# Kernel tuning notes

Measured on AMD Instinct MI355X. Metric: run time of the kernel, lower is better.

## Reference

```python
import jax, jax.numpy as jnp
import numpy as np

B, S, IN_DIM, OUT_DIM = 4, 8192, 1024, 1024


def setup_inputs() -> dict:
    key = jax.random.key(0)
    kx, km, kv, kt = jax.random.split(key, 4)
    x = jax.random.normal(kx, (B, S, IN_DIM), dtype=jnp.float32)
    visual_mask = jax.random.randint(km, (B, S), 0, 2) > 0  # bool [B, S]
    # nn.Linear(in_dim, out_dim, bias=False): weight shape [out_dim, in_dim]
    bound = 1.0 / np.sqrt(IN_DIM)
    W_v = jax.random.uniform(kv, (OUT_DIM, IN_DIM), dtype=jnp.float32, minval=-bound, maxval=bound)
    W_t = jax.random.uniform(kt, (OUT_DIM, IN_DIM), dtype=jnp.float32, minval=-bound, maxval=bound)
    return {"x": x, "visual_mask": visual_mask, "W_v": W_v, "W_t": W_t}


def reference(x, visual_mask, W_v, W_t):
    # out = linear_v(x) * mask + linear_t(x) * ~mask
    y_v = jnp.einsum("bsd,od->bso", x, W_v)  # [B, S, OUT_DIM]
    y_t = jnp.einsum("bsd,od->bso", x, W_t)
    m = visual_mask[:, :, None]  # [B, S, 1]
    return jnp.where(m, y_v, y_t)
```

## Files before the change

### kernel.cpp

```cpp
#include <hip/hip_runtime.h>
#include <hip/hip_bf16.h>
#include <stdint.h>

#define M_TOT  32768
#define K_DIM  1024
#define N_DIM  1024

typedef short bf16x8 __attribute__((ext_vector_type(8)));
typedef float f32x4  __attribute__((ext_vector_type(4)));

#define AS1(p) ((__attribute__((address_space(1))) void*)(p))
#define AS3(p) ((__attribute__((address_space(3))) void*)(p))

__device__ __forceinline__ uint32_t packbf2(float a, float b) {
    __hip_bfloat162 h = __float22bfloat162_rn(make_float2(a, b));
    union { __hip_bfloat162 h; uint32_t u; } cvt;
    cvt.h = h;
    return cvt.u;
}

__global__ __launch_bounds__(1024) void prep_kernel(
        const float* __restrict__ x,  const int* __restrict__ mask,
        const float* __restrict__ wv, const float* __restrict__ wt,
        ushort* __restrict__ xb, ushort* __restrict__ dv, ushort* __restrict__ dt,
        int* __restrict__ V, int* __restrict__ T, int* __restrict__ cnt) {
    const int b   = blockIdx.x;
    const int tid = threadIdx.x;

    if (b < 32) {
        const int lane = tid & 63;
        const int wv_i = tid >> 6;

        int pre = 0;
        const int nPre4 = b * 256;
        for (int i = tid; i < nPre4; i += 1024) {
            int4 v = ((const int4*)mask)[i];
            pre += (v.x != 0) + (v.y != 0) + (v.z != 0) + (v.w != 0);
        }
#pragma unroll
        for (int d = 32; d > 0; d >>= 1) pre += __shfl_down(pre, d);
        __shared__ int wsum[16];
        __shared__ int pref_s;
        if (lane == 0) wsum[wv_i] = pre;
        __syncthreads();
        if (tid == 0) {
            int s = 0;
#pragma unroll
            for (int i = 0; i < 16; ++i) s += wsum[i];
            pref_s = s;
        }
        __syncthreads();
        const int prefix_v = pref_s;

        const int e   = b * 1024 + tid;
        const int bit = (mask[e] != 0) ? 1 : 0;
        unsigned long long bal = __ballot(bit);
        const int lexcl = __popcll(bal & ((1ull << lane) - 1ull));
        const int wcnt  = __popcll(bal);
        __shared__ int wc[16];
        if (lane == 0) wc[wv_i] = wcnt;
        __syncthreads();
        int wpre = 0;
        for (int i = 0; i < wv_i; ++i) wpre += wc[i];
        int chunk_tot = 0;
#pragma unroll
        for (int i = 0; i < 16; ++i) chunk_tot += wc[i];
        const int gv = prefix_v + wpre + lexcl;
        if (bit) V[gv]     = e;
        else     T[e - gv] = e;

        if (b == 31) {
            const int Nv = prefix_v + chunk_tot;
            const int Nt = M_TOT - Nv;
            if (tid == 0) { cnt[0] = Nv; cnt[1] = Nt; }
            const int NBv = (Nv + 127) >> 7, NBt = (Nt + 127) >> 7;
            for (int p = Nv + tid; p < NBv * 128; p += 1024) V[p] = -1;
            for (int p = Nt + tid; p < NBt * 128; p += 1024) T[p] = -1;
        }
        return;
    }

    if (b < 288) {
        int u = (b - 32) * 8192 + tid * 8;
        const float* src; ushort* dst; int off;
        if (u < 1048576) { src = wv; dst = dv; off = u; }
        else             { src = wt; dst = dt; off = u - 1048576; }
        float4 a0 = *(const float4*)(src + off);
        float4 a1 = *(const float4*)(src + off + 4);
        uint4 p;
        p.x = packbf2(a0.x, a0.y);
        p.y = packbf2(a0.z, a0.w);
        p.z = packbf2(a1.x, a1.y);
        p.w = packbf2(a1.z, a1.w);
        *(uint4*)(dst + off) = p;
        return;
    }

    const int off = (b - 288) * 8192 + tid * 8;
    float4 a0 = *(const float4*)(x + off);
    float4 a1 = *(const float4*)(x + off + 4);
    uint4 p;
    p.x = packbf2(a0.x, a0.y);
    p.y = packbf2(a0.z, a0.w);
    p.z = packbf2(a1.x, a1.y);
    p.w = packbf2(a1.z, a1.w);
    *(uint4*)(xb + off) = p;
}

__global__ __launch_bounds__(256) void gemm_kernel(
        const ushort* __restrict__ xb,
        const ushort* __restrict__ Wv,
        const ushort* __restrict__ Wt,
        const int*    __restrict__ V,
        const int*    __restrict__ T,
        const int*    __restrict__ cnt,
        float*        __restrict__ out) {
    __shared__ ushort sA[128 * 64];
    __shared__ ushort sB[128 * 64];

    const int tid  = threadIdx.x;
    const int lane = tid & 63;
    const int w    = tid >> 6;

    const int kx = blockIdx.x & 7;
    const int bn = (blockIdx.x >> 3) & 7;
    const int gk = blockIdx.x >> 6;
    const int bm = gk * 8 + kx;

    const int Nv  = cnt[0];
    const int Nt  = cnt[1];
    const int NBv = (Nv + 127) >> 7;
    const int NBt = (Nt + 127) >> 7;
    if (bm >= NBv + NBt) return;

    const bool vis = (bm < NBv);
    const int*    rowbase = vis ? (V + (size_t)bm * 128)
                                : (T + (size_t)(bm - NBv) * 128);
    const ushort* W       = vis ? Wv : Wt;
    const int n0 = bn * 128;

    const int trow = tid >> 3;
    const int kcb  = (tid & 7) ^ (trow & 7);
    const ushort* ap[4];
    const ushort* wp[4];
#pragma unroll
    for (int r = 0; r < 4; ++r) {
        int rr = rowbase[r * 32 + trow];
        if (rr < 0) rr = 0;
        ap[r] = xb + (size_t)rr * K_DIM + kcb * 8;
        wp[r] = W + (size_t)(n0 + r * 32 + trow) * K_DIM + kcb * 8;
    }

    const int ml   = lane & 15;
    const int quad = lane >> 4;
    const int wm = (w & 1) * 64;
    const int wn = (w >> 1) * 64;
    uint32_t aoff[2][4], boff[2][4];
#pragma unroll
    for (int ks = 0; ks < 2; ++ks) {
        int kxr = (ks * 4 + quad) ^ (ml & 7);
#pragma unroll
        for (int t = 0; t < 4; ++t) {
            aoff[ks][t] = (uint32_t)(((wm + t * 16 + ml) * 8 + kxr) * 16);
            boff[ks][t] = (uint32_t)(((wn + t * 16 + ml) * 8 + kxr) * 16);
        }
    }

    f32x4 acc[4][4];
#pragma unroll
    for (int i = 0; i < 4; ++i)
#pragma unroll
        for (int j = 0; j < 4; ++j) {
            f32x4 z = {0.f, 0.f, 0.f, 0.f};
            acc[i][j] = z;
        }

    char* sAb = (char*)sA;
    char* sBb = (char*)sB;

    for (int kt = 0; kt < 16; ++kt) {
        const int k0 = kt * 64;
#pragma unroll
        for (int r = 0; r < 4; ++r) {
            char* lb = sBb + (size_t)(r * 256 + w * 64) * 16;
            __builtin_amdgcn_global_load_lds(AS1(wp[r] + k0), AS3(lb), 16, 0, 0);
        }
#pragma unroll
        for (int r = 0; r < 4; ++r) {
            char* la = sAb + (size_t)(r * 256 + w * 64) * 16;
            __builtin_amdgcn_global_load_lds(AS1(ap[r] + k0), AS3(la), 16, 0, 0);
        }
        __syncthreads();
#pragma unroll
        for (int ks = 0; ks < 2; ++ks) {
            bf16x8 af[4], bf[4];
#pragma unroll
            for (int t = 0; t < 4; ++t) af[t] = *(const bf16x8*)(sAb + aoff[ks][t]);
#pragma unroll
            for (int t = 0; t < 4; ++t) bf[t] = *(const bf16x8*)(sBb + boff[ks][t]);
#pragma unroll
            for (int tm = 0; tm < 4; ++tm)
#pragma unroll
                for (int tn = 0; tn < 4; ++tn)
                    acc[tm][tn] = __builtin_amdgcn_mfma_f32_16x16x32_bf16(
                        af[tm], bf[tn], acc[tm][tn], 0, 0, 0);
        }
        __syncthreads();
    }

#pragma unroll
    for (int tm = 0; tm < 4; ++tm) {
        const int rb = wm + tm * 16 + quad * 4;
        int sr0 = rowbase[rb + 0];
        int sr1 = rowbase[rb + 1];
        int sr2 = rowbase[rb + 2];
        int sr3 = rowbase[rb + 3];
#pragma unroll
        for (int tn = 0; tn < 4; ++tn) {
            const int col = n0 + wn + tn * 16 + ml;
            if (sr0 >= 0) out[(size_t)sr0 * N_DIM + col] = acc[tm][tn][0];
            if (sr1 >= 0) out[(size_t)sr1 * N_DIM + col] = acc[tm][tn][1];
            if (sr2 >= 0) out[(size_t)sr2 * N_DIM + col] = acc[tm][tn][2];
            if (sr3 >= 0) out[(size_t)sr3 * N_DIM + col] = acc[tm][tn][3];
        }
    }
}

extern "C" void kernel_launch(void* const* d_in, const int* in_sizes, int n_in,
                              void* d_out, int out_size, void* d_ws, size_t ws_size,
                              hipStream_t stream) {
    const float* x    = (const float*)d_in[0];
    const int*   mask = (const int*)d_in[1];
    const float* Wv   = (const float*)d_in[2];
    const float* Wt   = (const float*)d_in[3];
    float* out = (float*)d_out;

    char* ws = (char*)d_ws;
    ushort* xb  = (ushort*)(ws);
    ushort* dWv = (ushort*)(ws + 67108864);
    ushort* dWt = (ushort*)(ws + 69206016);
    int* V   = (int*)(ws + 71303168);
    int* T   = V + 32768;
    int* cnt = T + 32768;

    prep_kernel<<<4384, 1024, 0, stream>>>(x, mask, Wv, Wt, xb, dWv, dWt, V, T, cnt);
    gemm_kernel<<<33 * 64, 256, 0, stream>>>(xb, dWv, dWt, V, T, cnt, out);
}
```

Before: 341.5 us.

## Fuse activation bf16 conversion into GEMM by loading fp32 x directly

After: 380.4 us. 11.4% more time.

```diff
diff --git a/kernel.cpp b/kernel.cpp
--- a/kernel.cpp
+++ b/kernel.cpp
@@ -20,9 +20,9 @@
 }
 
 __global__ __launch_bounds__(1024) void prep_kernel(
-        const float* __restrict__ x,  const int* __restrict__ mask,
+        const int* __restrict__ mask,
         const float* __restrict__ wv, const float* __restrict__ wt,
-        ushort* __restrict__ xb, ushort* __restrict__ dv, ushort* __restrict__ dt,
+        ushort* __restrict__ dv, ushort* __restrict__ dt,
         int* __restrict__ V, int* __restrict__ T, int* __restrict__ cnt) {
     const int b   = blockIdx.x;
     const int tid = threadIdx.x;
@@ -80,42 +80,29 @@
         return;
     }
 
-    if (b < 288) {
-        int u = (b - 32) * 8192 + tid * 8;
-        const float* src; ushort* dst; int off;
-        if (u < 1048576) { src = wv; dst = dv; off = u; }
-        else             { src = wt; dst = dt; off = u - 1048576; }
-        float4 a0 = *(const float4*)(src + off);
-        float4 a1 = *(const float4*)(src + off + 4);
-        uint4 p;
-        p.x = packbf2(a0.x, a0.y);
-        p.y = packbf2(a0.z, a0.w);
-        p.z = packbf2(a1.x, a1.y);
-        p.w = packbf2(a1.z, a1.w);
-        *(uint4*)(dst + off) = p;
-        return;
-    }
-
-    const int off = (b - 288) * 8192 + tid * 8;
-    float4 a0 = *(const float4*)(x + off);
-    float4 a1 = *(const float4*)(x + off + 4);
+    int u = (b - 32) * 8192 + tid * 8;
+    const float* src; ushort* dst; int off;
+    if (u < 1048576) { src = wv; dst = dv; off = u; }
+    else             { src = wt; dst = dt; off = u - 1048576; }
+    float4 a0 = *(const float4*)(src + off);
+    float4 a1 = *(const float4*)(src + off + 4);
     uint4 p;
     p.x = packbf2(a0.x, a0.y);
     p.y = packbf2(a0.z, a0.w);
     p.z = packbf2(a1.x, a1.y);
     p.w = packbf2(a1.z, a1.w);
-    *(uint4*)(xb + off) = p;
+    *(uint4*)(dst + off) = p;
 }
 
 __global__ __launch_bounds__(256) void gemm_kernel(
-        const ushort* __restrict__ xb,
+        const float*  __restrict__ x,
         const ushort* __restrict__ Wv,
         const ushort* __restrict__ Wt,
         const int*    __restrict__ V,
         const int*    __restrict__ T,
         const int*    __restrict__ cnt,
         float*        __restrict__ out) {
-    __shared__ ushort sA[128 * 64];
+    __shared__ float  sA[128 * 64];
     __shared__ ushort sB[128 * 64];
 
     const int tid  = threadIdx.x;
@@ -139,15 +126,20 @@
     const ushort* W       = vis ? Wv : Wt;
     const int n0 = bn * 128;
 
+    const int arow = tid >> 4;
+    const int akc  = (tid & 15) ^ arow;
+    const float* ap8[8];
+#pragma unroll
+    for (int r = 0; r < 8; ++r) {
+        int rr = rowbase[r * 16 + arow];
+        if (rr < 0) rr = 0;
+        ap8[r] = x + (size_t)rr * K_DIM + akc * 4;
+    }
     const int trow = tid >> 3;
     const int kcb  = (tid & 7) ^ (trow & 7);
-    const ushort* ap[4];
     const ushort* wp[4];
 #pragma unroll
     for (int r = 0; r < 4; ++r) {
-        int rr = rowbase[r * 32 + trow];
-        if (rr < 0) rr = 0;
-        ap[r] = xb + (size_t)rr * K_DIM + kcb * 8;
         wp[r] = W + (size_t)(n0 + r * 32 + trow) * K_DIM + kcb * 8;
     }
 
@@ -158,10 +150,11 @@
     uint32_t aoff[2][4], boff[2][4];
 #pragma unroll
     for (int ks = 0; ks < 2; ++ks) {
-        int kxr = (ks * 4 + quad) ^ (ml & 7);
+        const int kc0 = ks * 8 + quad * 2;
+        const int kxr = (ks * 4 + quad) ^ (ml & 7);
 #pragma unroll
         for (int t = 0; t < 4; ++t) {
-            aoff[ks][t] = (uint32_t)(((wm + t * 16 + ml) * 8 + kxr) * 16);
+            aoff[ks][t] = (uint32_t)(((wm + t * 16 + ml) * 16 + (kc0 ^ ml)) * 16);
             boff[ks][t] = (uint32_t)(((wn + t * 16 + ml) * 8 + kxr) * 16);
         }
     }
@@ -186,16 +179,25 @@
             __builtin_amdgcn_global_load_lds(AS1(wp[r] + k0), AS3(lb), 16, 0, 0);
         }
 #pragma unroll
-        for (int r = 0; r < 4; ++r) {
+        for (int r = 0; r < 8; ++r) {
             char* la = sAb + (size_t)(r * 256 + w * 64) * 16;
-            __builtin_amdgcn_global_load_lds(AS1(ap[r] + k0), AS3(la), 16, 0, 0);
+            __builtin_amdgcn_global_load_lds(AS1(ap8[r] + k0), AS3(la), 16, 0, 0);
         }
         __syncthreads();
 #pragma unroll
         for (int ks = 0; ks < 2; ++ks) {
             bf16x8 af[4], bf[4];
 #pragma unroll
-            for (int t = 0; t < 4; ++t) af[t] = *(const bf16x8*)(sAb + aoff[ks][t]);
+            for (int t = 0; t < 4; ++t) {
+                f32x4 lo = *(const f32x4*)(sAb + aoff[ks][t]);
+                f32x4 hi = *(const f32x4*)(sAb + (aoff[ks][t] ^ 16u));
+                union { uint32_t u[4]; bf16x8 v; } cv;
+                cv.u[0] = packbf2(lo[0], lo[1]);
+                cv.u[1] = packbf2(lo[2], lo[3]);
+                cv.u[2] = packbf2(hi[0], hi[1]);
+                cv.u[3] = packbf2(hi[2], hi[3]);
+                af[t] = cv.v;
+            }
 #pragma unroll
             for (int t = 0; t < 4; ++t) bf[t] = *(const bf16x8*)(sBb + boff[ks][t]);
 #pragma unroll
@@ -236,13 +238,12 @@
     float* out = (float*)d_out;
 
     char* ws = (char*)d_ws;
-    ushort* xb  = (ushort*)(ws);
-    ushort* dWv = (ushort*)(ws + 67108864);
-    ushort* dWt = (ushort*)(ws + 69206016);
-    int* V   = (int*)(ws + 71303168);
+    ushort* dWv = (ushort*)(ws);
+    ushort* dWt = (ushort*)(ws + (1 << 21));
+    int* V   = (int*)(ws + (1 << 22));
     int* T   = V + 32768;
     int* cnt = T + 32768;
 
-    prep_kernel<<<4384, 1024, 0, stream>>>(x, mask, Wv, Wt, xb, dWv, dWt, V, T, cnt);
-    gemm_kernel<<<33 * 64, 256, 0, stream>>>(xb, dWv, dWt, V, T, cnt, out);
-}
+    prep_kernel<<<288, 1024, 0, stream>>>(mask, Wv, Wt, dWv, dWt, V, T, cnt);
+    gemm_kernel<<<33 * 64, 256, 0, stream>>>(x, dWv, dWt, V, T, cnt, out);
+}
```

## Enlarge GEMM tiles to 256x256 with double-buffered async LDS loads

Applied to the files above, without the earlier changes.

Result: faster. 324.1 us (-5.1%).

```diff
diff --git a/kernel.cpp b/kernel.cpp
--- a/kernel.cpp
+++ b/kernel.cpp
@@ -73,9 +73,9 @@
             const int Nv = prefix_v + chunk_tot;
             const int Nt = M_TOT - Nv;
             if (tid == 0) { cnt[0] = Nv; cnt[1] = Nt; }
-            const int NBv = (Nv + 127) >> 7, NBt = (Nt + 127) >> 7;
-            for (int p = Nv + tid; p < NBv * 128; p += 1024) V[p] = -1;
-            for (int p = Nt + tid; p < NBt * 128; p += 1024) T[p] = -1;
+            const int NBv = (Nv + 255) >> 8, NBt = (Nt + 255) >> 8;
+            for (int p = Nv + tid; p < NBv * 256; p += 1024) V[p] = -1;
+            for (int p = Nt + tid; p < NBt * 256; p += 1024) T[p] = -1;
         }
         return;
     }
@@ -107,7 +107,7 @@
     *(uint4*)(xb + off) = p;
 }
 
-__global__ __launch_bounds__(256) void gemm_kernel(
+__global__ __launch_bounds__(512, 2) void gemm_kernel(
         const ushort* __restrict__ xb,
         const ushort* __restrict__ Wv,
         const ushort* __restrict__ Wt,
@@ -115,29 +115,28 @@
         const int*    __restrict__ T,
         const int*    __restrict__ cnt,
         float*        __restrict__ out) {
-    __shared__ ushort sA[128 * 64];
-    __shared__ ushort sB[128 * 64];
+    __shared__ ushort sA[2][256 * 64];
+    __shared__ ushort sB[2][256 * 64];
 
     const int tid  = threadIdx.x;
     const int lane = tid & 63;
     const int w    = tid >> 6;
 
-    const int kx = blockIdx.x & 7;
-    const int bn = (blockIdx.x >> 3) & 7;
-    const int gk = blockIdx.x >> 6;
-    const int bm = gk * 8 + kx;
+    const int bid = blockIdx.x;
+    const int bm  = (bid & 7) + 8 * (bid >> 5);
+    const int bn  = (bid >> 3) & 3;
 
     const int Nv  = cnt[0];
     const int Nt  = cnt[1];
-    const int NBv = (Nv + 127) >> 7;
-    const int NBt = (Nt + 127) >> 7;
+    const int NBv = (Nv + 255) >> 8;
+    const int NBt = (Nt + 255) >> 8;
     if (bm >= NBv + NBt) return;
 
     const bool vis = (bm < NBv);
-    const int*    rowbase = vis ? (V + (size_t)bm * 128)
-                                : (T + (size_t)(bm - NBv) * 128);
+    const int*    rowbase = vis ? (V + (size_t)bm * 256)
+                                : (T + (size_t)(bm - NBv) * 256);
     const ushort* W       = vis ? Wv : Wt;
-    const int n0 = bn * 128;
+    const int n0 = bn * 256;
 
     const int trow = tid >> 3;
     const int kcb  = (tid & 7) ^ (trow & 7);
@@ -145,79 +144,108 @@
     const ushort* wp[4];
 #pragma unroll
     for (int r = 0; r < 4; ++r) {
-        int rr = rowbase[r * 32 + trow];
+        int rr = rowbase[r * 64 + trow];
         if (rr < 0) rr = 0;
         ap[r] = xb + (size_t)rr * K_DIM + kcb * 8;
-        wp[r] = W + (size_t)(n0 + r * 32 + trow) * K_DIM + kcb * 8;
+        wp[r] = W + (size_t)(n0 + r * 64 + trow) * K_DIM + kcb * 8;
     }
 
     const int ml   = lane & 15;
     const int quad = lane >> 4;
-    const int wm = (w & 1) * 64;
-    const int wn = (w >> 1) * 64;
-    uint32_t aoff[2][4], boff[2][4];
-#pragma unroll
-    for (int ks = 0; ks < 2; ++ks) {
-        int kxr = (ks * 4 + quad) ^ (ml & 7);
-#pragma unroll
-        for (int t = 0; t < 4; ++t) {
-            aoff[ks][t] = (uint32_t)(((wm + t * 16 + ml) * 8 + kxr) * 16);
-            boff[ks][t] = (uint32_t)(((wn + t * 16 + ml) * 8 + kxr) * 16);
-        }
-    }
-
-    f32x4 acc[4][4];
-#pragma unroll
-    for (int i = 0; i < 4; ++i)
+    const int wr = w >> 2;
+    const int wc = w & 3;
+    uint32_t aoff[8], boff[4];
+#pragma unroll
+    for (int t = 0; t < 8; ++t) {
+        const int am = wr * 128 + t * 16 + ml;
+        aoff[t] = (uint32_t)((am * 8 + (quad ^ (ml & 7))) * 16);
+    }
+#pragma unroll
+    for (int t = 0; t < 4; ++t) {
+        const int an = wc * 64 + t * 16 + ml;
+        boff[t] = (uint32_t)((an * 8 + (quad ^ (ml & 7))) * 16);
+    }
+
+    f32x4 acc[8][4];
+#pragma unroll
+    for (int i = 0; i < 8; ++i)
 #pragma unroll
         for (int j = 0; j < 4; ++j) {
             f32x4 z = {0.f, 0.f, 0.f, 0.f};
             acc[i][j] = z;
         }
 
-    char* sAb = (char*)sA;
-    char* sBb = (char*)sB;
-
-    for (int kt = 0; kt < 16; ++kt) {
-        const int k0 = kt * 64;
-#pragma unroll
-        for (int r = 0; r < 4; ++r) {
-            char* lb = sBb + (size_t)(r * 256 + w * 64) * 16;
-            __builtin_amdgcn_global_load_lds(AS1(wp[r] + k0), AS3(lb), 16, 0, 0);
-        }
-#pragma unroll
-        for (int r = 0; r < 4; ++r) {
-            char* la = sAb + (size_t)(r * 256 + w * 64) * 16;
-            __builtin_amdgcn_global_load_lds(AS1(ap[r] + k0), AS3(la), 16, 0, 0);
-        }
-        __syncthreads();
-#pragma unroll
-        for (int ks = 0; ks < 2; ++ks) {
-            bf16x8 af[4], bf[4];
-#pragma unroll
-            for (int t = 0; t < 4; ++t) af[t] = *(const bf16x8*)(sAb + aoff[ks][t]);
-#pragma unroll
-            for (int t = 0; t < 4; ++t) bf[t] = *(const bf16x8*)(sBb + boff[ks][t]);
-#pragma unroll
-            for (int tm = 0; tm < 4; ++tm)
-#pragma unroll
-                for (int tn = 0; tn < 4; ++tn)
-                    acc[tm][tn] = __builtin_amdgcn_mfma_f32_16x16x32_bf16(
-                        af[tm], bf[tn], acc[tm][tn], 0, 0, 0);
-        }
-        __syncthreads();
-    }
-
-#pragma unroll
-    for (int tm = 0; tm < 4; ++tm) {
-        const int rb = wm + tm * 16 + quad * 4;
+    char* a0 = (char*)sA[0];
+    char* a1 = (char*)sA[1];
+    char* b0 = (char*)sB[0];
+    char* b1 = (char*)sB[1];
+
+#define STAGE(AB, BB, T_)                                                         \
+    {                                                                             \
+        const int kk = (T_) * 64;                                                 \
+        _Pragma("unroll")                                                         \
+        for (int r = 0; r < 4; ++r) {                                             \
+            char* la = (AB) + (size_t)(r * 512 + w * 64) * 16;                    \
+            __builtin_amdgcn_global_load_lds(AS1(ap[r] + kk), AS3(la), 16, 0, 0); \
+        }                                                                         \
+        _Pragma("unroll")                                                         \
+        for (int r = 0; r < 4; ++r) {                                             \
+            char* lb = (BB) + (size_t)(r * 512 + w * 64) * 16;                    \
+            __builtin_amdgcn_global_load_lds(AS1(wp[r] + kk), AS3(lb), 16, 0, 0); \
+        }                                                                         \
+    }
+
+#define COMPUTE(AB, BB)                                                           \
+    {                                                                             \
+        _Pragma("unroll")                                                         \
+        for (int ksb = 0; ksb < 2; ++ksb) {                                       \
+            const uint32_t kx_ = (uint32_t)(ksb * 64);                            \
+            bf16x8 af[8], bf[4];                                                  \
+            _Pragma("unroll")                                                     \
+            for (int t = 0; t < 8; ++t) af[t] = *(const bf16x8*)((AB) + (aoff[t] ^ kx_)); \
+            _Pragma("unroll")                                                     \
+            for (int t = 0; t < 4; ++t) bf[t] = *(const bf16x8*)((BB) + (boff[t] ^ kx_)); \
+            _Pragma("unroll")                                                     \
+            for (int tm = 0; tm < 8; ++tm)                                        \
+                _Pragma("unroll")                                                 \
+                for (int tn = 0; tn < 4; ++tn)                                    \
+                    acc[tm][tn] = __builtin_amdgcn_mfma_f32_16x16x32_bf16(        \
+                        af[tm], bf[tn], acc[tm][tn], 0, 0, 0);                    \
+        }                                                                         \
+    }
+
+#define WAIT8 asm volatile("s_waitcnt vmcnt(8)" ::: "memory")
+#define WAIT0 asm volatile("s_waitcnt vmcnt(0)" ::: "memory")
+#define BAR   do { asm volatile("" ::: "memory"); __builtin_amdgcn_s_barrier(); \
+                   asm volatile("" ::: "memory"); } while (0)
+
+    WAIT0;
+    STAGE(a0, b0, 0);
+
+    for (int it = 0; it < 7; ++it) {
+        const int t0 = it * 2;
+        STAGE(a1, b1, t0 + 1); WAIT8; BAR; COMPUTE(a0, b0); BAR;
+        STAGE(a0, b0, t0 + 2); WAIT8; BAR; COMPUTE(a1, b1); BAR;
+    }
+    STAGE(a1, b1, 15); WAIT8; BAR; COMPUTE(a0, b0); BAR;
+    WAIT0; BAR; COMPUTE(a1, b1);
+
+#undef STAGE
+#undef COMPUTE
+#undef WAIT8
+#undef WAIT0
+#undef BAR
+
+#pragma unroll
+    for (int tm = 0; tm < 8; ++tm) {
+        const int rb = wr * 128 + tm * 16 + quad * 4;
         int sr0 = rowbase[rb + 0];
         int sr1 = rowbase[rb + 1];
         int sr2 = rowbase[rb + 2];
         int sr3 = rowbase[rb + 3];
 #pragma unroll
         for (int tn = 0; tn < 4; ++tn) {
-            const int col = n0 + wn + tn * 16 + ml;
+            const int col = n0 + wc * 64 + tn * 16 + ml;
             if (sr0 >= 0) out[(size_t)sr0 * N_DIM + col] = acc[tm][tn][0];
             if (sr1 >= 0) out[(size_t)sr1 * N_DIM + col] = acc[tm][tn][1];
             if (sr2 >= 0) out[(size_t)sr2 * N_DIM + col] = acc[tm][tn][2];
@@ -240,9 +268,9 @@
     ushort* dWv = (ushort*)(ws + 67108864);
     ushort* dWt = (ushort*)(ws + 69206016);
     int* V   = (int*)(ws + 71303168);
-    int* T   = V + 32768;
-    int* cnt = T + 32768;
+    int* T   = (int*)(ws + 71303168 + 132096);
+    int* cnt = (int*)(ws + 71303168 + 2 * 132096);
 
     prep_kernel<<<4384, 1024, 0, stream>>>(x, mask, Wv, Wt, xb, dWv, dWt, V, T, cnt);
-    gemm_kernel<<<33 * 64, 256, 0, stream>>>(xb, dWv, dWt, V, T, cnt, out);
-}
+    gemm_kernel<<<544, 512, 0, stream>>>(xb, dWv, dWt, V, T, cnt, out);
+}
```
